# Performance work log

Hardware: AMD Instinct MI355X
Metric: run time of the kernel (lower is better)

Reference implementation:

```python
import jax, jax.numpy as jnp
import numpy as np
import math

EMB_ATOM = 256
PAIR_IN = 64
PAIR_OUT = 64
EMB_RBF = 16
N_ATOMS = 50000
N_EDGES = 1_600_000
KMAX = 32


def setup_inputs() -> dict:
    key = jax.random.key(0)
    ks = jax.random.split(key, 8)
    h = jax.random.normal(ks[0], (N_ATOMS, EMB_ATOM), dtype=jnp.float32)
    rad_basis = jax.random.normal(ks[1], (N_ATOMS, EMB_RBF, KMAX), dtype=jnp.float32)
    edge_index = jax.random.randint(ks[2], (2, N_EDGES), 0, N_ATOMS, dtype=jnp.int64)
    target_neighbor_idx = jax.random.randint(ks[3], (N_EDGES,), 0, KMAX, dtype=jnp.int64)
    # Learned parameters (Dense layers are bias-free); stored as [in, out].
    W_down = jax.random.normal(ks[4], (EMB_ATOM, PAIR_IN), dtype=jnp.float32) / math.sqrt(EMB_ATOM)
    W_bilinear = jax.random.normal(ks[5], (EMB_RBF * PAIR_IN, PAIR_OUT), dtype=jnp.float32) / math.sqrt(EMB_RBF * PAIR_IN)
    W_up = jax.random.normal(ks[6], (PAIR_OUT, EMB_ATOM), dtype=jnp.float32) / math.sqrt(PAIR_OUT)
    scale = jnp.ones((), dtype=jnp.float32)  # ScaleFactor learned scalar
    return {"h": h, "rad_basis": rad_basis, "edge_index": edge_index,
            "target_neighbor_idx": target_neighbor_idx, "W_down": W_down,
            "W_bilinear": W_bilinear, "W_up": W_up, "scale": scale}


def reference(h, rad_basis, edge_index, target_neighbor_idx, W_down, W_bilinear, W_up, scale):
    num_atoms = h.shape[0]
    kmax = rad_basis.shape[-1]
    pair_in = W_down.shape[-1]
    # down_projection (Dense, silu activation, no bias)
    x_b = jax.nn.silu(h @ W_down)                              # [N, pair_in]
    x_ba = x_b[edge_index[0]]                                  # [E, pair_in] gather by source atom
    # scatter edge features into padded per-atom neighbor buffer
    x2 = jnp.zeros((num_atoms, kmax, pair_in), dtype=x_ba.dtype)
    x2 = x2.at[edge_index[1], target_neighbor_idx].set(x_ba)   # [N, Kmax, pair_in]
    # rbf-weighted neighbor aggregation: batched matmul
    x_ba2 = jnp.einsum('nrk,nkd->nrd', rad_basis, x2)          # [N, rbf, pair_in]
    h_out = x_ba2.reshape(num_atoms, -1) @ W_bilinear          # bilinear Dense, no activation
    h_out = h_out * scale                                      # ScaleFactor
    return jax.nn.silu(h_out @ W_up)                           # up_projection
```

## Files before the change

### kernel.cpp

```cpp
#include <hip/hip_runtime.h>

typedef __attribute__((ext_vector_type(8))) short short8;
typedef __attribute__((ext_vector_type(4))) float floatx4;
typedef unsigned short u16;

#define KMAXN 32

__device__ __forceinline__ u16 f2b(float f) {
    unsigned u = __builtin_bit_cast(unsigned, f);
    u += 0x7FFFu + ((u >> 16) & 1u);
    return (u16)(u >> 16);
}
__device__ __forceinline__ float silu_f(float x) {
    return x / (1.f + __expf(-x));
}

__global__ __launch_bounds__(256) void k_down(const float* __restrict__ h,
                                              const float* __restrict__ Wd,
                                              u16* __restrict__ xb) {
    const int tid  = threadIdx.x;
    const int wave = tid >> 6;
    const int lane = tid & 63;
    const int m = lane & 15;
    const int q = lane >> 4;
    const long atom0 = (long)blockIdx.x * 16;

    const float* arow = h + (atom0 + m) * 256 + q * 8;
    floatx4 acc = {0.f, 0.f, 0.f, 0.f};
#pragma unroll
    for (int kk = 0; kk < 8; ++kk) {
        float4 f0 = *reinterpret_cast<const float4*>(arow + kk * 32);
        float4 f1 = *reinterpret_cast<const float4*>(arow + kk * 32 + 4);
        short8 a;
        a[0] = (short)f2b(f0.x); a[1] = (short)f2b(f0.y);
        a[2] = (short)f2b(f0.z); a[3] = (short)f2b(f0.w);
        a[4] = (short)f2b(f1.x); a[5] = (short)f2b(f1.y);
        a[6] = (short)f2b(f1.z); a[7] = (short)f2b(f1.w);
        short8 b;
#pragma unroll
        for (int j = 0; j < 8; ++j) {
            int k = kk * 32 + q * 8 + j;
            b[j] = (short)f2b(Wd[k * 64 + wave * 16 + m]);
        }
        acc = __builtin_amdgcn_mfma_f32_16x16x32_bf16(a, b, acc, 0, 0, 0);
    }
#pragma unroll
    for (int r = 0; r < 4; ++r) {
        int row = q * 4 + r;
        xb[(atom0 + row) * 64 + wave * 16 + m] = f2b(silu_f(acc[r]));
    }
}

__global__ __launch_bounds__(256) void k_winner(const int* __restrict__ edst,
                                                const int* __restrict__ tni,
                                                int* __restrict__ winner, int E) {
    int e = blockIdx.x * 256 + threadIdx.x;
    if (e < E) {
        atomicMax(&winner[edst[e] * KMAXN + tni[e]], e);
    }
}

#define TL_STRIDE 1032

__global__ __launch_bounds__(256) void k_fused(
        const float* __restrict__ rad,
        const u16*   __restrict__ xb,
        const int*   __restrict__ winner,
        const int*   __restrict__ esrc,
        const float* __restrict__ Wb,
        const float* __restrict__ Wu,
        const float* __restrict__ scale_p,
        float* __restrict__ out) {
    __shared__ alignas(16) u16 t_lds[16][TL_STRIDE];
    __shared__ alignas(16) u16 c2_lds[16][72];
    __shared__ alignas(16) u16 x2s[4][KMAXN][64];

    const int tid  = threadIdx.x;
    const int wave = tid >> 6;
    const int lane = tid & 63;
    const int m = lane & 15;
    const int q = lane >> 4;
    const long atom0 = (long)blockIdx.x * 16;

    for (int a = 0; a < 4; ++a) {
        const long n = atom0 + wave * 4 + a;

        {
            int slot = lane >> 1;
            int half = lane & 1;
            int w = winner[n * KMAXN + slot];
            uint4 v0 = {0, 0, 0, 0}, v1 = {0, 0, 0, 0};
            uint4 v2 = {0, 0, 0, 0}, v3 = {0, 0, 0, 0};
            if (w >= 0) {
                int src = esrc[w];
                const uint4* p = reinterpret_cast<const uint4*>(xb + (long)src * 64 + half * 32);
                v0 = p[0]; v1 = p[1]; v2 = p[2]; v3 = p[3];
            }
            uint4* d = reinterpret_cast<uint4*>(&x2s[wave][slot][half * 32]);
            d[0] = v0; d[1] = v1; d[2] = v2; d[3] = v3;
        }
        __syncthreads();

        const float* rrow = rad + n * 512 + m * 32 + q * 8;
        float4 r0 = *reinterpret_cast<const float4*>(rrow);
        float4 r1 = *reinterpret_cast<const float4*>(rrow + 4);
        short8 ra;
        ra[0] = (short)f2b(r0.x); ra[1] = (short)f2b(r0.y);
        ra[2] = (short)f2b(r0.z); ra[3] = (short)f2b(r0.w);
        ra[4] = (short)f2b(r1.x); ra[5] = (short)f2b(r1.y);
        ra[6] = (short)f2b(r1.z); ra[7] = (short)f2b(r1.w);

#pragma unroll
        for (int c = 0; c < 4; ++c) {
            short8 bx;
#pragma unroll
            for (int j = 0; j < 8; ++j) {
                bx[j] = (short)x2s[wave][q * 8 + j][c * 16 + m];
            }
            floatx4 tz = {0.f, 0.f, 0.f, 0.f};
            tz = __builtin_amdgcn_mfma_f32_16x16x32_bf16(ra, bx, tz, 0, 0, 0);
#pragma unroll
            for (int r = 0; r < 4; ++r) {
                int rbf = q * 4 + r;
                t_lds[wave * 4 + a][rbf * 64 + c * 16 + m] = f2b(tz[r]);
            }
        }
        __syncthreads();
    }

    floatx4 c2 = {0.f, 0.f, 0.f, 0.f};
    for (int kk = 0; kk < 32; ++kk) {
        short8 af = *reinterpret_cast<const short8*>(&t_lds[m][kk * 32 + q * 8]);
        short8 bf;
#pragma unroll
        for (int j = 0; j < 8; ++j) {
            int k = kk * 32 + q * 8 + j;
            bf[j] = (short)f2b(Wb[k * 64 + wave * 16 + m]);
        }
        c2 = __builtin_amdgcn_mfma_f32_16x16x32_bf16(af, bf, c2, 0, 0, 0);
    }
    {
        float sc = scale_p[0];
#pragma unroll
        for (int r = 0; r < 4; ++r) {
            c2_lds[q * 4 + r][wave * 16 + m] = f2b(c2[r] * sc);
        }
    }
    __syncthreads();

#pragma unroll
    for (int tt = 0; tt < 4; ++tt) {
        floatx4 acc = {0.f, 0.f, 0.f, 0.f};
#pragma unroll
        for (int ks = 0; ks < 2; ++ks) {
            short8 af = *reinterpret_cast<const short8*>(&c2_lds[m][ks * 32 + q * 8]);
            short8 bf;
#pragma unroll
            for (int j = 0; j < 8; ++j) {
                int k = ks * 32 + q * 8 + j;
                bf[j] = (short)f2b(Wu[k * 256 + wave * 64 + tt * 16 + m]);
            }
            acc = __builtin_amdgcn_mfma_f32_16x16x32_bf16(af, bf, acc, 0, 0, 0);
        }
#pragma unroll
        for (int r = 0; r < 4; ++r) {
            int row = q * 4 + r;
            out[(atom0 + row) * 256 + wave * 64 + tt * 16 + m] = silu_f(acc[r]);
        }
    }
}

extern "C" void kernel_launch(void* const* d_in, const int* in_sizes, int n_in,
                              void* d_out, int out_size, void* d_ws, size_t ws_size,
                              hipStream_t stream) {
    const float* h     = (const float*)d_in[0];
    const float* rad   = (const float*)d_in[1];
    const int*   eidx  = (const int*)d_in[2];
    const int*   tni   = (const int*)d_in[3];
    const float* Wd    = (const float*)d_in[4];
    const float* Wb    = (const float*)d_in[5];
    const float* Wu    = (const float*)d_in[6];
    const float* scale = (const float*)d_in[7];
    float* out         = (float*)d_out;

    const int E = in_sizes[3];
    const int N = in_sizes[0] / 256;

    u16* xb = (u16*)d_ws;
    size_t xb_bytes = (size_t)N * 64 * sizeof(u16);
    int* winner = (int*)((char*)d_ws + xb_bytes);

    hipMemsetAsync(winner, 0xFF, (size_t)N * KMAXN * sizeof(int), stream);
    k_down<<<N / 16, 256, 0, stream>>>(h, Wd, xb);
    k_winner<<<(E + 255) / 256, 256, 0, stream>>>(eidx + E, tni, winner, E);
    k_fused<<<N / 16, 256, 0, stream>>>(rad, xb, winner, eidx, Wb, Wu, scale, out);
}
```

Baseline: 399.3 us.

## Pre-transpose weights to bf16, merge down/winner kernels, resolve sources, batch gathers

```diff
diff --git a/kernel.cpp b/kernel.cpp
--- a/kernel.cpp
+++ b/kernel.cpp
@@ -3,6 +3,7 @@
 typedef __attribute__((ext_vector_type(8))) short short8;
 typedef __attribute__((ext_vector_type(4))) float floatx4;
 typedef unsigned short u16;
+typedef unsigned long long u64;
 
 #define KMAXN 32
 
@@ -15,10 +16,37 @@
     return x / (1.f + __expf(-x));
 }
 
-__global__ __launch_bounds__(256) void k_down(const float* __restrict__ h,
-                                              const float* __restrict__ Wd,
-                                              u16* __restrict__ xb) {
-    const int tid  = threadIdx.x;
+__global__ __launch_bounds__(256) void k_xpose(const float* __restrict__ Wd,
+                                               const float* __restrict__ Wb,
+                                               const float* __restrict__ Wu,
+                                               u16* __restrict__ WdT,
+                                               u16* __restrict__ WbT,
+                                               u16* __restrict__ WuT) {
+    int idx = blockIdx.x * 256 + threadIdx.x;
+    if (idx < 16384) {
+        WdT[idx] = f2b(Wd[(idx & 255) * 64 + (idx >> 8)]);
+    } else if (idx < 81920) {
+        int i = idx - 16384;
+        WbT[i] = f2b(Wb[(i & 1023) * 64 + (i >> 10)]);
+    } else {
+        int i = idx - 81920;
+        WuT[i] = f2b(Wu[(i & 63) * 256 + (i >> 6)]);
+    }
+}
+
+__global__ __launch_bounds__(256) void k_prep(const float* __restrict__ h,
+                                              const u16*   __restrict__ WdT,
+                                              u16*         __restrict__ xb,
+                                              const int*   __restrict__ edst,
+                                              const int*   __restrict__ tni,
+                                              int*         __restrict__ winner,
+                                              int E, int DOWN) {
+    const int tid = threadIdx.x;
+    if ((int)blockIdx.x >= DOWN) {
+        int e = (blockIdx.x - DOWN) * 256 + tid;
+        if (e < E) atomicMax(&winner[edst[e] * KMAXN + tni[e]], e);
+        return;
+    }
     const int wave = tid >> 6;
     const int lane = tid & 63;
     const int m = lane & 15;
@@ -26,6 +54,7 @@
     const long atom0 = (long)blockIdx.x * 16;
 
     const float* arow = h + (atom0 + m) * 256 + q * 8;
+    const u16* brow = WdT + (wave * 16 + m) * 256 + q * 8;
     floatx4 acc = {0.f, 0.f, 0.f, 0.f};
 #pragma unroll
     for (int kk = 0; kk < 8; ++kk) {
@@ -36,12 +65,7 @@
         a[2] = (short)f2b(f0.z); a[3] = (short)f2b(f0.w);
         a[4] = (short)f2b(f1.x); a[5] = (short)f2b(f1.y);
         a[6] = (short)f2b(f1.z); a[7] = (short)f2b(f1.w);
-        short8 b;
-#pragma unroll
-        for (int j = 0; j < 8; ++j) {
-            int k = kk * 32 + q * 8 + j;
-            b[j] = (short)f2b(Wd[k * 64 + wave * 16 + m]);
-        }
+        short8 b = *reinterpret_cast<const short8*>(brow + kk * 32);
         acc = __builtin_amdgcn_mfma_f32_16x16x32_bf16(a, b, acc, 0, 0, 0);
     }
 #pragma unroll
@@ -51,29 +75,34 @@
     }
 }
 
-__global__ __launch_bounds__(256) void k_winner(const int* __restrict__ edst,
-                                                const int* __restrict__ tni,
-                                                int* __restrict__ winner, int E) {
-    int e = blockIdx.x * 256 + threadIdx.x;
-    if (e < E) {
-        atomicMax(&winner[edst[e] * KMAXN + tni[e]], e);
+__global__ __launch_bounds__(256) void k_resolve(int* __restrict__ winner,
+                                                 const int* __restrict__ esrc,
+                                                 int n4) {
+    int i = blockIdx.x * 256 + threadIdx.x;
+    if (i < n4) {
+        int4 w = reinterpret_cast<int4*>(winner)[i];
+        w.x = (w.x >= 0) ? esrc[w.x] : -1;
+        w.y = (w.y >= 0) ? esrc[w.y] : -1;
+        w.z = (w.z >= 0) ? esrc[w.z] : -1;
+        w.w = (w.w >= 0) ? esrc[w.w] : -1;
+        reinterpret_cast<int4*>(winner)[i] = w;
     }
 }
 
 #define TL_STRIDE 1032
+#define X2_PAD    68
 
 __global__ __launch_bounds__(256) void k_fused(
         const float* __restrict__ rad,
         const u16*   __restrict__ xb,
         const int*   __restrict__ winner,
-        const int*   __restrict__ esrc,
-        const float* __restrict__ Wb,
-        const float* __restrict__ Wu,
+        const u16*   __restrict__ WbT,
+        const u16*   __restrict__ WuT,
         const float* __restrict__ scale_p,
         float* __restrict__ out) {
     __shared__ alignas(16) u16 t_lds[16][TL_STRIDE];
     __shared__ alignas(16) u16 c2_lds[16][72];
-    __shared__ alignas(16) u16 x2s[4][KMAXN][64];
+    __shared__ alignas(16) u16 x2s[4][KMAXN][X2_PAD];
 
     const int tid  = threadIdx.x;
     const int wave = tid >> 6;
@@ -81,34 +110,46 @@
     const int m = lane & 15;
     const int q = lane >> 4;
     const long atom0 = (long)blockIdx.x * 16;
-
+    const long nbase = atom0 + wave * 4;
+
+    const int slot = lane >> 1;
+    const int half = lane & 1;
+
+    int src[4];
+#pragma unroll
+    for (int a = 0; a < 4; ++a) src[a] = winner[(nbase + a) * KMAXN + slot];
+
+    short8 ra[4];
+#pragma unroll
     for (int a = 0; a < 4; ++a) {
-        const long n = atom0 + wave * 4 + a;
-
-        {
-            int slot = lane >> 1;
-            int half = lane & 1;
-            int w = winner[n * KMAXN + slot];
-            uint4 v0 = {0, 0, 0, 0}, v1 = {0, 0, 0, 0};
-            uint4 v2 = {0, 0, 0, 0}, v3 = {0, 0, 0, 0};
-            if (w >= 0) {
-                int src = esrc[w];
-                const uint4* p = reinterpret_cast<const uint4*>(xb + (long)src * 64 + half * 32);
-                v0 = p[0]; v1 = p[1]; v2 = p[2]; v3 = p[3];
-            }
-            uint4* d = reinterpret_cast<uint4*>(&x2s[wave][slot][half * 32]);
-            d[0] = v0; d[1] = v1; d[2] = v2; d[3] = v3;
-        }
-        __syncthreads();
-
-        const float* rrow = rad + n * 512 + m * 32 + q * 8;
+        const float* rrow = rad + (nbase + a) * 512 + m * 32 + q * 8;
         float4 r0 = *reinterpret_cast<const float4*>(rrow);
         float4 r1 = *reinterpret_cast<const float4*>(rrow + 4);
-        short8 ra;
-        ra[0] = (short)f2b(r0.x); ra[1] = (short)f2b(r0.y);
-        ra[2] = (short)f2b(r0.z); ra[3] = (short)f2b(r0.w);
-        ra[4] = (short)f2b(r1.x); ra[5] = (short)f2b(r1.y);
-        ra[6] = (short)f2b(r1.z); ra[7] = (short)f2b(r1.w);
+        ra[a][0] = (short)f2b(r0.x); ra[a][1] = (short)f2b(r0.y);
+        ra[a][2] = (short)f2b(r0.z); ra[a][3] = (short)f2b(r0.w);
+        ra[a][4] = (short)f2b(r1.x); ra[a][5] = (short)f2b(r1.y);
+        ra[a][6] = (short)f2b(r1.z); ra[a][7] = (short)f2b(r1.w);
+    }
+
+    uint4 g[4][4];
+#pragma unroll
+    for (int a = 0; a < 4; ++a) {
+        if (src[a] >= 0) {
+            const uint4* p = reinterpret_cast<const uint4*>(xb + (long)src[a] * 64 + half * 32);
+            g[a][0] = p[0]; g[a][1] = p[1]; g[a][2] = p[2]; g[a][3] = p[3];
+        } else {
+            uint4 z = {0, 0, 0, 0};
+            g[a][0] = z; g[a][1] = z; g[a][2] = z; g[a][3] = z;
+        }
+    }
+
+#pragma unroll
+    for (int a = 0; a < 4; ++a) {
+        u64* d = reinterpret_cast<u64*>(&x2s[wave][slot][half * 32]);
+        const u64* s = reinterpret_cast<const u64*>(&g[a][0]);
+#pragma unroll
+        for (int i = 0; i < 8; ++i) d[i] = s[i];
+        asm volatile("s_waitcnt lgkmcnt(0)" ::: "memory");
 
 #pragma unroll
         for (int c = 0; c < 4; ++c) {
@@ -118,25 +159,22 @@
                 bx[j] = (short)x2s[wave][q * 8 + j][c * 16 + m];
             }
             floatx4 tz = {0.f, 0.f, 0.f, 0.f};
-            tz = __builtin_amdgcn_mfma_f32_16x16x32_bf16(ra, bx, tz, 0, 0, 0);
+            tz = __builtin_amdgcn_mfma_f32_16x16x32_bf16(ra[a], bx, tz, 0, 0, 0);
 #pragma unroll
             for (int r = 0; r < 4; ++r) {
-                int rbf = q * 4 + r;
-                t_lds[wave * 4 + a][rbf * 64 + c * 16 + m] = f2b(tz[r]);
+                t_lds[wave * 4 + a][(q * 4 + r) * 64 + c * 16 + m] = f2b(tz[r]);
             }
         }
-        __syncthreads();
-    }
+        asm volatile("" ::: "memory");
+    }
+    __syncthreads();
 
     floatx4 c2 = {0.f, 0.f, 0.f, 0.f};
+    const u16* wbrow = WbT + (wave * 16 + m) * 1024 + q * 8;
+#pragma unroll 4
     for (int kk = 0; kk < 32; ++kk) {
         short8 af = *reinterpret_cast<const short8*>(&t_lds[m][kk * 32 + q * 8]);
-        short8 bf;
-#pragma unroll
-        for (int j = 0; j < 8; ++j) {
-            int k = kk * 32 + q * 8 + j;
-            bf[j] = (short)f2b(Wb[k * 64 + wave * 16 + m]);
-        }
+        short8 bf = *reinterpret_cast<const short8*>(wbrow + kk * 32);
         c2 = __builtin_amdgcn_mfma_f32_16x16x32_bf16(af, bf, c2, 0, 0, 0);
     }
     {
@@ -151,21 +189,16 @@
 #pragma unroll
     for (int tt = 0; tt < 4; ++tt) {
         floatx4 acc = {0.f, 0.f, 0.f, 0.f};
+        const u16* wurow = WuT + (wave * 64 + tt * 16 + m) * 64 + q * 8;
 #pragma unroll
         for (int ks = 0; ks < 2; ++ks) {
             short8 af = *reinterpret_cast<const short8*>(&c2_lds[m][ks * 32 + q * 8]);
-            short8 bf;
-#pragma unroll
-            for (int j = 0; j < 8; ++j) {
-                int k = ks * 32 + q * 8 + j;
-                bf[j] = (short)f2b(Wu[k * 256 + wave * 64 + tt * 16 + m]);
-            }
+            short8 bf = *reinterpret_cast<const short8*>(wurow + ks * 32);
             acc = __builtin_amdgcn_mfma_f32_16x16x32_bf16(af, bf, acc, 0, 0, 0);
         }
 #pragma unroll
         for (int r = 0; r < 4; ++r) {
-            int row = q * 4 + r;
-            out[(atom0 + row) * 256 + wave * 64 + tt * 16 + m] = silu_f(acc[r]);
+            out[(atom0 + q * 4 + r) * 256 + wave * 64 + tt * 16 + m] = silu_f(acc[r]);
         }
     }
 }
@@ -187,11 +220,20 @@
     const int N = in_sizes[0] / 256;
 
     u16* xb = (u16*)d_ws;
-    size_t xb_bytes = (size_t)N * 64 * sizeof(u16);
-    int* winner = (int*)((char*)d_ws + xb_bytes);
+    size_t off = (size_t)N * 64 * sizeof(u16);
+    int* winner = (int*)((char*)d_ws + off);
+    off += (size_t)N * KMAXN * sizeof(int);
+    u16* WdT = (u16*)((char*)d_ws + off);  off += 16384 * 2;
+    u16* WbT = (u16*)((char*)d_ws + off);  off += 65536 * 2;
+    u16* WuT = (u16*)((char*)d_ws + off);
+
+    const int DOWN = N / 16;
+    const int WIN  = (E + 255) / 256;
+    const int S4   = (N * KMAXN) / 4;
 
     hipMemsetAsync(winner, 0xFF, (size_t)N * KMAXN * sizeof(int), stream);
-    k_down<<<N / 16, 256, 0, stream>>>(h, Wd, xb);
-    k_winner<<<(E + 255) / 256, 256, 0, stream>>>(eidx + E, tni, winner, E);
-    k_fused<<<N / 16, 256, 0, stream>>>(rad, xb, winner, eidx, Wb, Wu, scale, out);
-}
+    k_xpose<<<384, 256, 0, stream>>>(Wd, Wb, Wu, WdT, WbT, WuT);
+    k_prep<<<DOWN + WIN, 256, 0, stream>>>(h, WdT, xb, eidx + E, tni, winner, E, DOWN);
+    k_resolve<<<(S4 + 255) / 256, 256, 0, stream>>>(winner, eidx, S4);
+    k_fused<<<DOWN, 256, 0, stream>>>(rad, xb, winner, WbT, WuT, scale, out);
+}
```

Measured after the change: 364.3 us. 8.8% less time.
